# Kernel optimization log

Hardware: AMD Instinct MI355X
Metric: run time of the kernel (lower is better)

The kernel has to match this reference:

```python
import jax, jax.numpy as jnp
import numpy as np

N_NODES = 50000
N_EDGES = 1000000
NODE_IN = 64
EDGE_OUT = 64
NODE_OUT = 64
GLOBAL_DIM = 64
N_GRAPHS = 64


def _glorot(key, shape):
    fan_in = shape[0]
    return (jax.random.normal(key, shape, dtype=jnp.float32) / jnp.sqrt(jnp.float32(fan_in)))


def setup_inputs() -> dict:
    key = jax.random.key(0)
    ks = jax.random.split(key, 12)
    x = jax.random.normal(ks[0], (N_NODES, NODE_IN), dtype=jnp.float32)
    edge_index = jax.random.randint(ks[1], (2, N_EDGES), 0, N_NODES, dtype=jnp.int64 if jax.config.jax_enable_x64 else jnp.int32)
    edge_attr = jax.random.normal(ks[2], (N_EDGES, EDGE_OUT), dtype=jnp.float32)
    u = jax.random.normal(ks[3], (N_GRAPHS, GLOBAL_DIM), dtype=jnp.float32)
    batch = jnp.sort(jax.random.randint(ks[4], (N_NODES,), 0, N_GRAPHS, dtype=jnp.int64 if jax.config.jax_enable_x64 else jnp.int32))
    # node_mlp_1: Linear(node_in+edge_out -> node_out), ReLU, Linear(node_out -> node_out)
    W1 = _glorot(ks[5], (NODE_IN + EDGE_OUT, NODE_OUT))
    b1 = jnp.zeros((NODE_OUT,), dtype=jnp.float32)
    W2 = _glorot(ks[6], (NODE_OUT, NODE_OUT))
    b2 = jnp.zeros((NODE_OUT,), dtype=jnp.float32)
    # node_mlp_2: Linear(global_dim+node_in+node_out -> node_out), ReLU, Linear(node_out -> node_out)
    W3 = _glorot(ks[7], (GLOBAL_DIM + NODE_IN + NODE_OUT, NODE_OUT))
    b3 = jnp.zeros((NODE_OUT,), dtype=jnp.float32)
    W4 = _glorot(ks[8], (NODE_OUT, NODE_OUT))
    b4 = jnp.zeros((NODE_OUT,), dtype=jnp.float32)
    return {"x": x, "edge_index": edge_index, "edge_attr": edge_attr, "u": u, "batch": batch,
            "W1": W1, "b1": b1, "W2": W2, "b2": b2, "W3": W3, "b3": b3, "W4": W4, "b4": b4}


def reference(x, edge_index, edge_attr, u, batch, W1, b1, W2, b2, W3, b3, W4, b4):
    row, col = edge_index[0], edge_index[1]
    # per-edge MLP on [x[row] || edge_attr]  -> [E, node_out]
    e = jnp.concatenate([x[row], edge_attr], axis=1)
    e = jnp.maximum(e @ W1 + b1, 0.0) @ W2 + b2
    # scatter_mean over destination nodes (zero where a node has no incoming edges)
    sums = jax.ops.segment_sum(e, col, num_segments=N_NODES)
    counts = jax.ops.segment_sum(jnp.ones((e.shape[0],), dtype=e.dtype), col, num_segments=N_NODES)
    agg = sums / jnp.clip(counts, 1.0)[:, None]
    # per-node MLP on [x || agg || u[batch]]
    h = jnp.concatenate([x, agg, u[batch]], axis=1)
    return jnp.maximum(h @ W3 + b3, 0.0) @ W4 + b4
```

## Files before the change

kernel.cpp:

```cpp
#include <hip/hip_runtime.h>

#define E_TOTAL 1000000
#define NN 50000
#define NB_SCAN ((NN + 255) / 256)

typedef __attribute__((ext_vector_type(8))) short bf16x8;
typedef __attribute__((ext_vector_type(8))) __bf16 bfv8;
typedef __attribute__((ext_vector_type(4))) float f32x4;
typedef __attribute__((ext_vector_type(8))) unsigned short u16x8;

__device__ __forceinline__ float bf2f(unsigned short u) {
  unsigned int x = ((unsigned int)u) << 16;
  return __builtin_bit_cast(float, x);
}

__device__ __forceinline__ unsigned short f2bf(float v) {
  __bf16 b = (__bf16)v;
  return __builtin_bit_cast(unsigned short, b);
}

__device__ __forceinline__ bf16x8 pack8(float4 u, float4 v) {
  bfv8 f;
  f[0] = (__bf16)u.x; f[1] = (__bf16)u.y; f[2] = (__bf16)u.z; f[3] = (__bf16)u.w;
  f[4] = (__bf16)v.x; f[5] = (__bf16)v.y; f[6] = (__bf16)v.z; f[7] = (__bf16)v.w;
  return __builtin_bit_cast(bf16x8, f);
}

__device__ __forceinline__ bf16x8 cvt8(const float* __restrict__ p) {
  return pack8(*reinterpret_cast<const float4*>(p), *reinterpret_cast<const float4*>(p + 4));
}

__device__ __forceinline__ bf16x8 cvt8s(const float* __restrict__ p, float s) {
  const float4 v0 = *reinterpret_cast<const float4*>(p);
  const float4 v1 = *reinterpret_cast<const float4*>(p + 4);
  bfv8 f;
  f[0] = (__bf16)(v0.x * s); f[1] = (__bf16)(v0.y * s); f[2] = (__bf16)(v0.z * s); f[3] = (__bf16)(v0.w * s);
  f[4] = (__bf16)(v1.x * s); f[5] = (__bf16)(v1.y * s); f[6] = (__bf16)(v1.z * s); f[7] = (__bf16)(v1.w * s);
  return __builtin_bit_cast(bf16x8, f);
}


__global__ void count_kernel(const int* __restrict__ ei, float* __restrict__ counts) {
  int i = blockIdx.x * blockDim.x + threadIdx.x;
  if (i < E_TOTAL) atomicAdd(counts + ei[E_TOTAL + i], 1.0f);
}

__global__ void hist_kernel(const int* __restrict__ ei, int* __restrict__ cnt) {
  int i = blockIdx.x * blockDim.x + threadIdx.x;
  if (i < E_TOTAL) atomicAdd(cnt + ei[E_TOTAL + i], 1);
}

__global__ void scan_block_kernel(const int* __restrict__ cnt, int* __restrict__ offs,
                                  int* __restrict__ btot) {
  __shared__ int s[256];
  const int tid = threadIdx.x;
  const int i = blockIdx.x * 256 + tid;
  int v = (i < NN) ? cnt[i] : 0;
  s[tid] = v;
  __syncthreads();
#pragma unroll
  for (int d = 1; d < 256; d <<= 1) {
    int t = (tid >= d) ? s[tid - d] : 0;
    __syncthreads();
    s[tid] += t;
    __syncthreads();
  }
  int incl = s[tid];
  if (i < NN) offs[i] = incl - v;
  if (tid == 255) btot[blockIdx.x] = incl;
}

__global__ void scan_add_kernel(int* __restrict__ offs, const int* __restrict__ btot,
                                int* __restrict__ run) {
  __shared__ int s[256];
  const int tid = threadIdx.x, bid = blockIdx.x;
  s[tid] = (tid < bid && tid < NB_SCAN) ? btot[tid] : 0;
  __syncthreads();
#pragma unroll
  for (int d = 128; d > 0; d >>= 1) {
    if (tid < d) s[tid] += s[tid + d];
    __syncthreads();
  }
  const int base = s[0];
  const int i = bid * 256 + tid;
  if (i < NN) {
    int o = offs[i] + base;
    offs[i] = o;
    run[i] = o;
  }
  if (i == 0) offs[NN] = E_TOTAL;
}

template <int MODE>
__global__ __launch_bounds__(512) void edge_kernel(
    const float* __restrict__ x, const int* __restrict__ ei,
    const float* __restrict__ ea, const float* __restrict__ W1,
    const float* __restrict__ b1, const float* __restrict__ W2,
    const float* __restrict__ b2, float* __restrict__ sums,
    unsigned short* __restrict__ hbuf, int* __restrict__ run) {
  __shared__ unsigned short wlds[24 * 512];
  __shared__ unsigned short h_lds[8][16 * 72];
  const int tid = threadIdx.x;
  const int w = tid >> 6, l = tid & 63;
  const int c = l & 15, g = l >> 4;

  for (int idx = tid; idx < 16 * 512; idx += 512) {
    const int e = idx & 7, ll = (idx >> 3) & 63, ft = idx >> 9;
    const int s = ft >> 2, t = ft & 3;
    wlds[idx] = f2bf(W1[(s * 32 + (ll >> 4) * 8 + e) * 64 + t * 16 + (ll & 15)]);
  }
  for (int idx = tid; idx < 8 * 512; idx += 512) {
    const int e = idx & 7, ll = (idx >> 3) & 63, ft = idx >> 9;
    const int s = ft >> 2, t = ft & 3;
    wlds[16 * 512 + idx] = f2bf(W2[(s * 32 + (ll >> 4) * 8 + e) * 64 + t * 16 + (ll & 15)]);
  }
  __syncthreads();

  const int ebase0 = blockIdx.x * 512 + w * 64;
  if (ebase0 >= E_TOTAL) return;

  float b1v[4], b2v[4];
#pragma unroll
  for (int t = 0; t < 4; ++t) {
    b1v[t] = b1[t * 16 + c];
    b2v[t] = b2[t * 16 + c];
  }
  unsigned short* hl = h_lds[w];

  int idxc = ei[ebase0 + c];
  int colc = (MODE == 1) ? ei[E_TOTAL + ebase0 + c] : 0;
  const float* xp0 = x + (long)idxc * 64 + g * 8;
  const float* ap0 = ea + (long)(ebase0 + c) * 64 + g * 8;
  float4 xc0 = *reinterpret_cast<const float4*>(xp0);
  float4 xc1 = *reinterpret_cast<const float4*>(xp0 + 4);
  float4 xc2 = *reinterpret_cast<const float4*>(xp0 + 32);
  float4 xc3 = *reinterpret_cast<const float4*>(xp0 + 36);
  float4 ac0 = *reinterpret_cast<const float4*>(ap0);
  float4 ac1 = *reinterpret_cast<const float4*>(ap0 + 4);
  float4 ac2 = *reinterpret_cast<const float4*>(ap0 + 32);
  float4 ac3 = *reinterpret_cast<const float4*>(ap0 + 36);

#pragma unroll 1
  for (int it = 0; it < 4; ++it) {
    const int ebc = ebase0 + it * 16;
    const bool hasnext = (it < 3);

    int posc = 0;
    if (MODE == 1 && g == 0) posc = atomicAdd(run + colc, 1);

    bf16x8 a0 = pack8(xc0, xc1);
    bf16x8 a1 = pack8(xc2, xc3);
    bf16x8 a2 = pack8(ac0, ac1);
    bf16x8 a3 = pack8(ac2, ac3);

    int idxn = 0, coln = 0;
    float4 an0, an1, an2, an3, xn0, xn1, xn2, xn3;
    if (hasnext) {
      idxn = ei[ebc + 16 + c];
      if (MODE == 1) coln = ei[E_TOTAL + ebc + 16 + c];
      const float* apn = ea + (long)(ebc + 16 + c) * 64 + g * 8;
      an0 = *reinterpret_cast<const float4*>(apn);
      an1 = *reinterpret_cast<const float4*>(apn + 4);
      an2 = *reinterpret_cast<const float4*>(apn + 32);
      an3 = *reinterpret_cast<const float4*>(apn + 36);
    }

    f32x4 acc[4];
#pragma unroll
    for (int t = 0; t < 4; ++t) acc[t] = (f32x4){0.f, 0.f, 0.f, 0.f};
#pragma unroll
    for (int t = 0; t < 4; ++t) {
      bf16x8 wf0 = *reinterpret_cast<const bf16x8*>(wlds + ((0 * 4 + t) * 64 + l) * 8);
      bf16x8 wf1 = *reinterpret_cast<const bf16x8*>(wlds + ((1 * 4 + t) * 64 + l) * 8);
      bf16x8 wf2 = *reinterpret_cast<const bf16x8*>(wlds + ((2 * 4 + t) * 64 + l) * 8);
      bf16x8 wf3 = *reinterpret_cast<const bf16x8*>(wlds + ((3 * 4 + t) * 64 + l) * 8);
      acc[t] = __builtin_amdgcn_mfma_f32_16x16x32_bf16(a0, wf0, acc[t], 0, 0, 0);
      acc[t] = __builtin_amdgcn_mfma_f32_16x16x32_bf16(a1, wf1, acc[t], 0, 0, 0);
      acc[t] = __builtin_amdgcn_mfma_f32_16x16x32_bf16(a2, wf2, acc[t], 0, 0, 0);
      acc[t] = __builtin_amdgcn_mfma_f32_16x16x32_bf16(a3, wf3, acc[t], 0, 0, 0);
    }

    if (hasnext) {
      const float* xpn = x + (long)idxn * 64 + g * 8;
      xn0 = *reinterpret_cast<const float4*>(xpn);
      xn1 = *reinterpret_cast<const float4*>(xpn + 4);
      xn2 = *reinterpret_cast<const float4*>(xpn + 32);
      xn3 = *reinterpret_cast<const float4*>(xpn + 36);
    }

#pragma unroll
    for (int t = 0; t < 4; ++t)
#pragma unroll
      for (int r = 0; r < 4; ++r)
        hl[(g * 4 + r) * 72 + t * 16 + c] = f2bf(fmaxf(acc[t][r] + b1v[t], 0.f));
    __builtin_amdgcn_wave_barrier();
    bf16x8 h0 = *reinterpret_cast<const bf16x8*>(hl + c * 72 + g * 8);
    bf16x8 h1 = *reinterpret_cast<const bf16x8*>(hl + c * 72 + 32 + g * 8);

    f32x4 o[4];
#pragma unroll
    for (int t = 0; t < 4; ++t) o[t] = (f32x4){0.f, 0.f, 0.f, 0.f};
#pragma unroll
    for (int t = 0; t < 4; ++t) {
      bf16x8 wf0 = *reinterpret_cast<const bf16x8*>(wlds + 16 * 512 + ((0 * 4 + t) * 64 + l) * 8);
      bf16x8 wf1 = *reinterpret_cast<const bf16x8*>(wlds + 16 * 512 + ((1 * 4 + t) * 64 + l) * 8);
      o[t] = __builtin_amdgcn_mfma_f32_16x16x32_bf16(h0, wf0, o[t], 0, 0, 0);
      o[t] = __builtin_amdgcn_mfma_f32_16x16x32_bf16(h1, wf1, o[t], 0, 0, 0);
    }
    __builtin_amdgcn_wave_barrier();

    if (MODE == 0) {
#pragma unroll
      for (int r = 0; r < 4; ++r) {
        const int node = ei[E_TOTAL + ebc + g * 4 + r];
#pragma unroll
        for (int t = 0; t < 4; ++t)
          atomicAdd(sums + (long)node * 64 + t * 16 + c, o[t][r] + b2v[t]);
      }
    } else {
#pragma unroll
      for (int t = 0; t < 4; ++t)
#pragma unroll
        for (int r = 0; r < 4; ++r)
          hl[(g * 4 + r) * 72 + t * 16 + c] = f2bf(o[t][r] + b2v[t]);
      __builtin_amdgcn_wave_barrier();
      {
        const int srow = l >> 2, k4 = l & 3;
        const int pos = __shfl(posc, srow);
        const unsigned short* src = hl + srow * 72 + k4 * 16;
        unsigned short* dst = hbuf + (size_t)pos * 64 + k4 * 16;
        u16x8 v0 = *reinterpret_cast<const u16x8*>(src);
        u16x8 v1 = *reinterpret_cast<const u16x8*>(src + 8);
        *reinterpret_cast<u16x8*>(dst) = v0;
        *reinterpret_cast<u16x8*>(dst + 8) = v1;
      }
      __builtin_amdgcn_wave_barrier();
    }

    if (hasnext) {
      xc0 = xn0; xc1 = xn1; xc2 = xn2; xc3 = xn3;
      ac0 = an0; ac1 = an1; ac2 = an2; ac3 = an3;
      colc = coln;
    }
  }
}

__global__ __launch_bounds__(256, 1) void reduce_kernel(
    const unsigned short* __restrict__ hbuf, const int* __restrict__ offs,
    float* __restrict__ out) {
  const int l = threadIdx.x & 63, w = threadIdx.x >> 6;
  const int n = blockIdx.x * 4 + w;
  if (n >= NN) return;
  const int start = offs[n], end = offs[n + 1];
  const int slot = l >> 3, ch8 = (l & 7) * 8;
  float acc[8];
#pragma unroll
  for (int k = 0; k < 8; ++k) acc[k] = 0.f;
  for (int j0 = start; j0 < end; j0 += 8) {
    const int j = j0 + slot;
    if (j < end) {
      u16x8 v = *reinterpret_cast<const u16x8*>(hbuf + (size_t)j * 64 + ch8);
#pragma unroll
      for (int k = 0; k < 8; ++k) acc[k] += bf2f(v[k]);
    }
  }
#pragma unroll
  for (int k = 0; k < 8; ++k) {
    float v = acc[k];
    v += __shfl_xor(v, 8);
    v += __shfl_xor(v, 16);
    v += __shfl_xor(v, 32);
    acc[k] = v;
  }
  if (l < 8) {
    const float inv = 1.0f / fmaxf((float)(end - start), 1.0f);
    float* op = out + (size_t)n * 64 + l * 8;
    float4 r0 = {acc[0] * inv, acc[1] * inv, acc[2] * inv, acc[3] * inv};
    float4 r1 = {acc[4] * inv, acc[5] * inv, acc[6] * inv, acc[7] * inv};
    *reinterpret_cast<float4*>(op) = r0;
    *reinterpret_cast<float4*>(op + 4) = r1;
  }
}

template <bool WITH_INV>
__global__ __launch_bounds__(256, 1) void node_kernel(
    const float* __restrict__ x, const int* __restrict__ batch,
    const float* __restrict__ u, const float* __restrict__ W3,
    const float* __restrict__ b3, const float* __restrict__ W4,
    const float* __restrict__ b4, const float* __restrict__ counts,
    float* __restrict__ out) {
  __shared__ unsigned short h_lds[4][16 * 72];
  const int tid = threadIdx.x;
  const int w = tid >> 6, l = tid & 63;
  const int c = l & 15, g = l >> 4;

  bf16x8 w3f[6][4];
#pragma unroll
  for (int s = 0; s < 6; ++s)
#pragma unroll
    for (int t = 0; t < 4; ++t) {
      const float* wp = W3 + (s * 32 + g * 8) * 64 + t * 16 + c;
      bfv8 f;
#pragma unroll
      for (int e = 0; e < 8; ++e) f[e] = (__bf16)wp[e * 64];
      w3f[s][t] = __builtin_bit_cast(bf16x8, f);
    }
  bf16x8 w4f[2][4];
#pragma unroll
  for (int s = 0; s < 2; ++s)
#pragma unroll
    for (int t = 0; t < 4; ++t) {
      const float* wp = W4 + (s * 32 + g * 8) * 64 + t * 16 + c;
      bfv8 f;
#pragma unroll
      for (int e = 0; e < 8; ++e) f[e] = (__bf16)wp[e * 64];
      w4f[s][t] = __builtin_bit_cast(bf16x8, f);
    }
  float b3v[4], b4v[4];
#pragma unroll
  for (int t = 0; t < 4; ++t) {
    b3v[t] = b3[t * 16 + c];
    b4v[t] = b4[t * 16 + c];
  }

  unsigned short* hl = h_lds[w];
  const int nbase0 = blockIdx.x * 256 + w * 64;
#pragma unroll 1
  for (int it = 0; it < 4; ++it) {
    const int nb = nbase0 + it * 16;
    if (nb >= NN) break;
    const int my_n = nb + c;
    const float* xp = x + (long)my_n * 64 + g * 8;
    const float* sp = out + (long)my_n * 64 + g * 8;
    const float* up = u + (long)batch[my_n] * 64 + g * 8;
    bf16x8 a0 = cvt8(xp);
    bf16x8 a1 = cvt8(xp + 32);
    bf16x8 a2, a3;
    if (WITH_INV) {
      const float inv = 1.0f / fmaxf(counts[my_n], 1.0f);
      a2 = cvt8s(sp, inv);
      a3 = cvt8s(sp + 32, inv);
    } else {
      a2 = cvt8(sp);
      a3 = cvt8(sp + 32);
    }
    bf16x8 a4 = cvt8(up);
    bf16x8 a5 = cvt8(up + 32);

    f32x4 acc[4];
#pragma unroll
    for (int t = 0; t < 4; ++t) acc[t] = (f32x4){0.f, 0.f, 0.f, 0.f};
#pragma unroll
    for (int t = 0; t < 4; ++t) {
      acc[t] = __builtin_amdgcn_mfma_f32_16x16x32_bf16(a0, w3f[0][t], acc[t], 0, 0, 0);
      acc[t] = __builtin_amdgcn_mfma_f32_16x16x32_bf16(a1, w3f[1][t], acc[t], 0, 0, 0);
      acc[t] = __builtin_amdgcn_mfma_f32_16x16x32_bf16(a2, w3f[2][t], acc[t], 0, 0, 0);
      acc[t] = __builtin_amdgcn_mfma_f32_16x16x32_bf16(a3, w3f[3][t], acc[t], 0, 0, 0);
      acc[t] = __builtin_amdgcn_mfma_f32_16x16x32_bf16(a4, w3f[4][t], acc[t], 0, 0, 0);
      acc[t] = __builtin_amdgcn_mfma_f32_16x16x32_bf16(a5, w3f[5][t], acc[t], 0, 0, 0);
    }
#pragma unroll
    for (int t = 0; t < 4; ++t)
#pragma unroll
      for (int r = 0; r < 4; ++r)
        hl[(g * 4 + r) * 72 + t * 16 + c] = f2bf(fmaxf(acc[t][r] + b3v[t], 0.f));
    __builtin_amdgcn_wave_barrier();
    bf16x8 h0 = *reinterpret_cast<const bf16x8*>(hl + c * 72 + g * 8);
    bf16x8 h1 = *reinterpret_cast<const bf16x8*>(hl + c * 72 + 32 + g * 8);
    f32x4 o[4];
#pragma unroll
    for (int t = 0; t < 4; ++t) o[t] = (f32x4){0.f, 0.f, 0.f, 0.f};
#pragma unroll
    for (int t = 0; t < 4; ++t) {
      o[t] = __builtin_amdgcn_mfma_f32_16x16x32_bf16(h0, w4f[0][t], o[t], 0, 0, 0);
      o[t] = __builtin_amdgcn_mfma_f32_16x16x32_bf16(h1, w4f[1][t], o[t], 0, 0, 0);
    }
    __builtin_amdgcn_wave_barrier();
#pragma unroll
    for (int r = 0; r < 4; ++r) {
      const int nrow = nb + g * 4 + r;
#pragma unroll
      for (int t = 0; t < 4; ++t)
        out[(long)nrow * 64 + t * 16 + c] = o[t][r] + b4v[t];
    }
  }
}

extern "C" void kernel_launch(void* const* d_in, const int* in_sizes, int n_in,
                              void* d_out, int out_size, void* d_ws, size_t ws_size,
                              hipStream_t stream) {
  const float* x = (const float*)d_in[0];
  const int* ei = (const int*)d_in[1];
  const float* ea = (const float*)d_in[2];
  const float* u = (const float*)d_in[3];
  const int* batch = (const int*)d_in[4];
  const float* W1 = (const float*)d_in[5];
  const float* b1 = (const float*)d_in[6];
  const float* W2 = (const float*)d_in[7];
  const float* b2 = (const float*)d_in[8];
  const float* W3 = (const float*)d_in[9];
  const float* b3 = (const float*)d_in[10];
  const float* W4 = (const float*)d_in[11];
  const float* b4 = (const float*)d_in[12];
  float* out = (float*)d_out;

  const size_t HB_OFF = 0;
  const size_t OFFS_OFF = 128000000;
  const size_t RUN_OFF = 128400000;
  const size_t BTOT_OFF = 128800000;
  const size_t NEED = 128900000;

  const int egrid = (E_TOTAL + 255) / 256;
  const int egrid512 = (E_TOTAL + 511) / 512;
  const int ngrid = (NN + 255) / 256;

  if (ws_size >= NEED) {
    unsigned short* hbuf = (unsigned short*)((char*)d_ws + HB_OFF);
    int* offs = (int*)((char*)d_ws + OFFS_OFF);
    int* run = (int*)((char*)d_ws + RUN_OFF);
    int* btot = (int*)((char*)d_ws + BTOT_OFF);

    hipMemsetAsync(run, 0, (size_t)NN * sizeof(int), stream);
    hist_kernel<<<egrid, 256, 0, stream>>>(ei, run);
    scan_block_kernel<<<NB_SCAN, 256, 0, stream>>>(run, offs, btot);
    scan_add_kernel<<<NB_SCAN, 256, 0, stream>>>(offs, btot, run);
    edge_kernel<1><<<egrid512, 512, 0, stream>>>(x, ei, ea, W1, b1, W2, b2, nullptr, hbuf, run);
    reduce_kernel<<<(NN + 3) / 4, 256, 0, stream>>>(hbuf, offs, out);
    node_kernel<false><<<ngrid, 256, 0, stream>>>(x, batch, u, W3, b3, W4, b4, nullptr, out);
  } else {
    float* counts = (float*)d_ws;
    hipMemsetAsync(out, 0, (size_t)NN * 64 * sizeof(float), stream);
    hipMemsetAsync(counts, 0, (size_t)NN * sizeof(float), stream);
    count_kernel<<<egrid, 256, 0, stream>>>(ei, counts);
    edge_kernel<0><<<egrid512, 512, 0, stream>>>(x, ei, ea, W1, b1, W2, b2, out, nullptr, nullptr);
    node_kernel<true><<<ngrid, 256, 0, stream>>>(x, batch, u, W3, b3, W4, b4, counts, out);
  }
}
```

Before: 228.0 us.

## Sort edges by destination and reduce runs in-register before atomic scatter

Edges are counting-sorted by destination into a compact struct array (src, edge id, dst), and the edge MLP then processes edges in sorted order. Same-destination edges are summed in registers, with a whole-wave shortcut when all 16 rows share a node, before fp32 atomics into a sums buffer. This removes the 128MB bf16 per-edge intermediate buffer and the separate reduce kernel. The cost is a scatter kernel, gathered (non-contiguous) edge_attr reads, and remaining atomics, and accumulation order now varies between runs.

```diff
diff --git a/kernel.cpp b/kernel.cpp
--- a/kernel.cpp
+++ b/kernel.cpp
@@ -7,12 +7,6 @@
 typedef __attribute__((ext_vector_type(8))) short bf16x8;
 typedef __attribute__((ext_vector_type(8))) __bf16 bfv8;
 typedef __attribute__((ext_vector_type(4))) float f32x4;
-typedef __attribute__((ext_vector_type(8))) unsigned short u16x8;
-
-__device__ __forceinline__ float bf2f(unsigned short u) {
-  unsigned int x = ((unsigned int)u) << 16;
-  return __builtin_bit_cast(float, x);
-}
 
 __device__ __forceinline__ unsigned short f2bf(float v) {
   __bf16 b = (__bf16)v;
@@ -39,11 +33,6 @@
   return __builtin_bit_cast(bf16x8, f);
 }
 
-
-__global__ void count_kernel(const int* __restrict__ ei, float* __restrict__ counts) {
-  int i = blockIdx.x * blockDim.x + threadIdx.x;
-  if (i < E_TOTAL) atomicAdd(counts + ei[E_TOTAL + i], 1.0f);
-}
 
 __global__ void hist_kernel(const int* __restrict__ ei, int* __restrict__ cnt) {
   int i = blockIdx.x * blockDim.x + threadIdx.x;
@@ -70,7 +59,7 @@
   if (tid == 255) btot[blockIdx.x] = incl;
 }
 
-__global__ void scan_add_kernel(int* __restrict__ offs, const int* __restrict__ btot,
+__global__ void scan_add_kernel(const int* __restrict__ offs_in, const int* __restrict__ btot,
                                 int* __restrict__ run) {
   __shared__ int s[256];
   const int tid = threadIdx.x, bid = blockIdx.x;
@@ -83,21 +72,25 @@
   }
   const int base = s[0];
   const int i = bid * 256 + tid;
-  if (i < NN) {
-    int o = offs[i] + base;
-    offs[i] = o;
-    run[i] = o;
-  }
-  if (i == 0) offs[NN] = E_TOTAL;
-}
-
-template <int MODE>
+  if (i < NN) run[i] = offs_in[i] + base;
+}
+
+__global__ void scatter_kernel(const int* __restrict__ ei, int* __restrict__ run,
+                               int4* __restrict__ structs) {
+  int i = blockIdx.x * blockDim.x + threadIdx.x;
+  if (i < E_TOTAL) {
+    const int src = ei[i];
+    const int dst = ei[E_TOTAL + i];
+    const int pos = atomicAdd(run + dst, 1);
+    structs[pos] = (int4){src, i, dst, 0};
+  }
+}
+
 __global__ __launch_bounds__(512) void edge_kernel(
-    const float* __restrict__ x, const int* __restrict__ ei,
+    const float* __restrict__ x, const int4* __restrict__ structs,
     const float* __restrict__ ea, const float* __restrict__ W1,
     const float* __restrict__ b1, const float* __restrict__ W2,
-    const float* __restrict__ b2, float* __restrict__ sums,
-    unsigned short* __restrict__ hbuf, int* __restrict__ run) {
+    const float* __restrict__ b2, float* __restrict__ sums) {
   __shared__ unsigned short wlds[24 * 512];
   __shared__ unsigned short h_lds[8][16 * 72];
   const int tid = threadIdx.x;
@@ -127,10 +120,14 @@
   }
   unsigned short* hl = h_lds[w];
 
-  int idxc = ei[ebase0 + c];
-  int colc = (MODE == 1) ? ei[E_TOTAL + ebase0 + c] : 0;
-  const float* xp0 = x + (long)idxc * 64 + g * 8;
-  const float* ap0 = ea + (long)(ebase0 + c) * 64 + g * 8;
+  int4 s0 = structs[ebase0 + c];
+  int4 s1 = structs[ebase0 + 16 + c];
+  {
+    const float* xp0 = x + (long)s0.x * 64 + g * 8;
+    const float* ap0 = ea + (long)s0.y * 64 + g * 8;
+  }
+  const float* xp0 = x + (long)s0.x * 64 + g * 8;
+  const float* ap0 = ea + (long)s0.y * 64 + g * 8;
   float4 xc0 = *reinterpret_cast<const float4*>(xp0);
   float4 xc1 = *reinterpret_cast<const float4*>(xp0 + 4);
   float4 xc2 = *reinterpret_cast<const float4*>(xp0 + 32);
@@ -145,25 +142,21 @@
     const int ebc = ebase0 + it * 16;
     const bool hasnext = (it < 3);
 
-    int posc = 0;
-    if (MODE == 1 && g == 0) posc = atomicAdd(run + colc, 1);
+    int4 s2 = (int4){0, 0, 0, 0};
+    float4 an0, an1, an2, an3, xn0, xn1, xn2, xn3;
+    if (hasnext) {
+      const float* apn = ea + (long)s1.y * 64 + g * 8;
+      an0 = *reinterpret_cast<const float4*>(apn);
+      an1 = *reinterpret_cast<const float4*>(apn + 4);
+      an2 = *reinterpret_cast<const float4*>(apn + 32);
+      an3 = *reinterpret_cast<const float4*>(apn + 36);
+      if (it < 2) s2 = structs[ebc + 32 + c];
+    }
 
     bf16x8 a0 = pack8(xc0, xc1);
     bf16x8 a1 = pack8(xc2, xc3);
     bf16x8 a2 = pack8(ac0, ac1);
     bf16x8 a3 = pack8(ac2, ac3);
-
-    int idxn = 0, coln = 0;
-    float4 an0, an1, an2, an3, xn0, xn1, xn2, xn3;
-    if (hasnext) {
-      idxn = ei[ebc + 16 + c];
-      if (MODE == 1) coln = ei[E_TOTAL + ebc + 16 + c];
-      const float* apn = ea + (long)(ebc + 16 + c) * 64 + g * 8;
-      an0 = *reinterpret_cast<const float4*>(apn);
-      an1 = *reinterpret_cast<const float4*>(apn + 4);
-      an2 = *reinterpret_cast<const float4*>(apn + 32);
-      an3 = *reinterpret_cast<const float4*>(apn + 36);
-    }
 
     f32x4 acc[4];
 #pragma unroll
@@ -181,7 +174,7 @@
     }
 
     if (hasnext) {
-      const float* xpn = x + (long)idxn * 64 + g * 8;
+      const float* xpn = x + (long)s1.x * 64 + g * 8;
       xn0 = *reinterpret_cast<const float4*>(xpn);
       xn1 = *reinterpret_cast<const float4*>(xpn + 4);
       xn2 = *reinterpret_cast<const float4*>(xpn + 32);
@@ -208,87 +201,55 @@
       o[t] = __builtin_amdgcn_mfma_f32_16x16x32_bf16(h1, wf1, o[t], 0, 0, 0);
     }
     __builtin_amdgcn_wave_barrier();
-
-    if (MODE == 0) {
-#pragma unroll
-      for (int r = 0; r < 4; ++r) {
-        const int node = ei[E_TOTAL + ebc + g * 4 + r];
-#pragma unroll
-        for (int t = 0; t < 4; ++t)
-          atomicAdd(sums + (long)node * 64 + t * 16 + c, o[t][r] + b2v[t]);
+#pragma unroll
+    for (int t = 0; t < 4; ++t)
+#pragma unroll
+      for (int r = 0; r < 4; ++r) o[t][r] += b2v[t];
+
+    const int d0 = __shfl(s0.z, 0);
+    const bool uni = __all(s0.z == d0);
+    if (uni) {
+#pragma unroll
+      for (int t = 0; t < 4; ++t) {
+        float s = o[t][0] + o[t][1] + o[t][2] + o[t][3];
+        s += __shfl_xor(s, 16);
+        s += __shfl_xor(s, 32);
+        if (l < 16) atomicAdd(sums + (long)d0 * 64 + t * 16 + c, s);
       }
     } else {
-#pragma unroll
-      for (int t = 0; t < 4; ++t)
-#pragma unroll
-        for (int r = 0; r < 4; ++r)
-          hl[(g * 4 + r) * 72 + t * 16 + c] = f2bf(o[t][r] + b2v[t]);
-      __builtin_amdgcn_wave_barrier();
-      {
-        const int srow = l >> 2, k4 = l & 3;
-        const int pos = __shfl(posc, srow);
-        const unsigned short* src = hl + srow * 72 + k4 * 16;
-        unsigned short* dst = hbuf + (size_t)pos * 64 + k4 * 16;
-        u16x8 v0 = *reinterpret_cast<const u16x8*>(src);
-        u16x8 v1 = *reinterpret_cast<const u16x8*>(src + 8);
-        *reinterpret_cast<u16x8*>(dst) = v0;
-        *reinterpret_cast<u16x8*>(dst + 8) = v1;
+      int n0 = __shfl(s0.z, 4 * g + 0);
+      int n1 = __shfl(s0.z, 4 * g + 1);
+      int n2 = __shfl(s0.z, 4 * g + 2);
+      int n3 = __shfl(s0.z, 4 * g + 3);
+#pragma unroll
+      for (int t = 0; t < 4; ++t) {
+        const int chb = t * 16 + c;
+        float acc2 = o[t][0];
+        int cur = n0;
+        if (n1 == cur) acc2 += o[t][1];
+        else { atomicAdd(sums + (long)cur * 64 + chb, acc2); acc2 = o[t][1]; cur = n1; }
+        if (n2 == cur) acc2 += o[t][2];
+        else { atomicAdd(sums + (long)cur * 64 + chb, acc2); acc2 = o[t][2]; cur = n2; }
+        if (n3 == cur) acc2 += o[t][3];
+        else { atomicAdd(sums + (long)cur * 64 + chb, acc2); acc2 = o[t][3]; cur = n3; }
+        atomicAdd(sums + (long)cur * 64 + chb, acc2);
       }
-      __builtin_amdgcn_wave_barrier();
     }
 
     if (hasnext) {
       xc0 = xn0; xc1 = xn1; xc2 = xn2; xc3 = xn3;
       ac0 = an0; ac1 = an1; ac2 = an2; ac3 = an3;
-      colc = coln;
-    }
-  }
-}
-
-__global__ __launch_bounds__(256, 1) void reduce_kernel(
-    const unsigned short* __restrict__ hbuf, const int* __restrict__ offs,
-    float* __restrict__ out) {
-  const int l = threadIdx.x & 63, w = threadIdx.x >> 6;
-  const int n = blockIdx.x * 4 + w;
-  if (n >= NN) return;
-  const int start = offs[n], end = offs[n + 1];
-  const int slot = l >> 3, ch8 = (l & 7) * 8;
-  float acc[8];
-#pragma unroll
-  for (int k = 0; k < 8; ++k) acc[k] = 0.f;
-  for (int j0 = start; j0 < end; j0 += 8) {
-    const int j = j0 + slot;
-    if (j < end) {
-      u16x8 v = *reinterpret_cast<const u16x8*>(hbuf + (size_t)j * 64 + ch8);
-#pragma unroll
-      for (int k = 0; k < 8; ++k) acc[k] += bf2f(v[k]);
-    }
-  }
-#pragma unroll
-  for (int k = 0; k < 8; ++k) {
-    float v = acc[k];
-    v += __shfl_xor(v, 8);
-    v += __shfl_xor(v, 16);
-    v += __shfl_xor(v, 32);
-    acc[k] = v;
-  }
-  if (l < 8) {
-    const float inv = 1.0f / fmaxf((float)(end - start), 1.0f);
-    float* op = out + (size_t)n * 64 + l * 8;
-    float4 r0 = {acc[0] * inv, acc[1] * inv, acc[2] * inv, acc[3] * inv};
-    float4 r1 = {acc[4] * inv, acc[5] * inv, acc[6] * inv, acc[7] * inv};
-    *reinterpret_cast<float4*>(op) = r0;
-    *reinterpret_cast<float4*>(op + 4) = r1;
-  }
-}
-
-template <bool WITH_INV>
+      s0 = s1; s1 = s2;
+    }
+  }
+}
+
 __global__ __launch_bounds__(256, 1) void node_kernel(
     const float* __restrict__ x, const int* __restrict__ batch,
     const float* __restrict__ u, const float* __restrict__ W3,
     const float* __restrict__ b3, const float* __restrict__ W4,
-    const float* __restrict__ b4, const float* __restrict__ counts,
-    float* __restrict__ out) {
+    const float* __restrict__ b4, const int* __restrict__ cnt,
+    const float* __restrict__ sums, float* __restrict__ out) {
   __shared__ unsigned short h_lds[4][16 * 72];
   const int tid = threadIdx.x;
   const int w = tid >> 6, l = tid & 63;
@@ -331,19 +292,13 @@
     if (nb >= NN) break;
     const int my_n = nb + c;
     const float* xp = x + (long)my_n * 64 + g * 8;
-    const float* sp = out + (long)my_n * 64 + g * 8;
+    const float* sp = sums + (long)my_n * 64 + g * 8;
     const float* up = u + (long)batch[my_n] * 64 + g * 8;
+    const float inv = 1.0f / fmaxf((float)cnt[my_n], 1.0f);
     bf16x8 a0 = cvt8(xp);
     bf16x8 a1 = cvt8(xp + 32);
-    bf16x8 a2, a3;
-    if (WITH_INV) {
-      const float inv = 1.0f / fmaxf(counts[my_n], 1.0f);
-      a2 = cvt8s(sp, inv);
-      a3 = cvt8s(sp + 32, inv);
-    } else {
-      a2 = cvt8(sp);
-      a3 = cvt8(sp + 32);
-    }
+    bf16x8 a2 = cvt8s(sp, inv);
+    bf16x8 a3 = cvt8s(sp + 32, inv);
     bf16x8 a4 = cvt8(up);
     bf16x8 a5 = cvt8(up + 32);
 
@@ -404,35 +359,30 @@
   const float* b4 = (const float*)d_in[12];
   float* out = (float*)d_out;
 
-  const size_t HB_OFF = 0;
-  const size_t OFFS_OFF = 128000000;
-  const size_t RUN_OFF = 128400000;
-  const size_t BTOT_OFF = 128800000;
-  const size_t NEED = 128900000;
+  const size_t ST_OFF = 0;
+  const size_t SUM_OFF = 16000000;
+  const size_t CNT_OFF = 28800000;
+  const size_t RUN_OFF = 29000000;
+  const size_t OFFS_OFF = 29200000;
+  const size_t BTOT_OFF = 29400000;
+
+  int4* structs = (int4*)((char*)d_ws + ST_OFF);
+  float* sums = (float*)((char*)d_ws + SUM_OFF);
+  int* cnt = (int*)((char*)d_ws + CNT_OFF);
+  int* run = (int*)((char*)d_ws + RUN_OFF);
+  int* offs = (int*)((char*)d_ws + OFFS_OFF);
+  int* btot = (int*)((char*)d_ws + BTOT_OFF);
 
   const int egrid = (E_TOTAL + 255) / 256;
   const int egrid512 = (E_TOTAL + 511) / 512;
   const int ngrid = (NN + 255) / 256;
 
-  if (ws_size >= NEED) {
-    unsigned short* hbuf = (unsigned short*)((char*)d_ws + HB_OFF);
-    int* offs = (int*)((char*)d_ws + OFFS_OFF);
-    int* run = (int*)((char*)d_ws + RUN_OFF);
-    int* btot = (int*)((char*)d_ws + BTOT_OFF);
-
-    hipMemsetAsync(run, 0, (size_t)NN * sizeof(int), stream);
-    hist_kernel<<<egrid, 256, 0, stream>>>(ei, run);
-    scan_block_kernel<<<NB_SCAN, 256, 0, stream>>>(run, offs, btot);
-    scan_add_kernel<<<NB_SCAN, 256, 0, stream>>>(offs, btot, run);
-    edge_kernel<1><<<egrid512, 512, 0, stream>>>(x, ei, ea, W1, b1, W2, b2, nullptr, hbuf, run);
-    reduce_kernel<<<(NN + 3) / 4, 256, 0, stream>>>(hbuf, offs, out);
-    node_kernel<false><<<ngrid, 256, 0, stream>>>(x, batch, u, W3, b3, W4, b4, nullptr, out);
-  } else {
-    float* counts = (float*)d_ws;
-    hipMemsetAsync(out, 0, (size_t)NN * 64 * sizeof(float), stream);
-    hipMemsetAsync(counts, 0, (size_t)NN * sizeof(float), stream);
-    count_kernel<<<egrid, 256, 0, stream>>>(ei, counts);
-    edge_kernel<0><<<egrid512, 512, 0, stream>>>(x, ei, ea, W1, b1, W2, b2, out, nullptr, nullptr);
-    node_kernel<true><<<ngrid, 256, 0, stream>>>(x, batch, u, W3, b3, W4, b4, counts, out);
-  }
-}
+  hipMemsetAsync(cnt, 0, (size_t)NN * sizeof(int), stream);
+  hipMemsetAsync(sums, 0, (size_t)NN * 64 * sizeof(float), stream);
+  hist_kernel<<<egrid, 256, 0, stream>>>(ei, cnt);
+  scan_block_kernel<<<NB_SCAN, 256, 0, stream>>>(cnt, offs, btot);
+  scan_add_kernel<<<NB_SCAN, 256, 0, stream>>>(offs, btot, run);
+  scatter_kernel<<<egrid, 256, 0, stream>>>(ei, run, structs);
+  edge_kernel<<<egrid512, 512, 0, stream>>>(x, structs, ea, W1, b1, W2, b2, sums);
+  node_kernel<<<ngrid, 256, 0, stream>>>(x, batch, u, W3, b3, W4, b4, cnt, sums, out);
+}
```

New measurement: 322.3 us. 1.41x slower.

## Fold edge second linear layer into node MLP weights, pre-convert x to bf16

Applied to the files above, without the earlier changes.

Because scatter-mean is linear, the second edge-MLP layer (W2, b2) is moved after aggregation. It is folded into W3 as W2·W3 plus a bias term that is applied only to nodes with incoming edges. The edge kernel now writes ReLU(first-layer) activations straight to the sorted buffer, which removes the second MFMA pass and the LDS round trip. A small kernel pre-converts x to bf16 to halve gather traffic. The code also drops the low-workspace fallback path and batches the atomic position reservation per wave. In exchange it adds two tiny launches and a precomputed weight product whose rounding differs slightly from the reference.

```diff
diff --git a/kernel.cpp b/kernel.cpp
--- a/kernel.cpp
+++ b/kernel.cpp
@@ -7,6 +7,7 @@
 typedef __attribute__((ext_vector_type(8))) short bf16x8;
 typedef __attribute__((ext_vector_type(8))) __bf16 bfv8;
 typedef __attribute__((ext_vector_type(4))) float f32x4;
+typedef __attribute__((ext_vector_type(4))) unsigned short u16x4;
 typedef __attribute__((ext_vector_type(8))) unsigned short u16x8;
 
 __device__ __forceinline__ float bf2f(unsigned short u) {
@@ -30,20 +31,37 @@
   return pack8(*reinterpret_cast<const float4*>(p), *reinterpret_cast<const float4*>(p + 4));
 }
 
-__device__ __forceinline__ bf16x8 cvt8s(const float* __restrict__ p, float s) {
-  const float4 v0 = *reinterpret_cast<const float4*>(p);
-  const float4 v1 = *reinterpret_cast<const float4*>(p + 4);
-  bfv8 f;
-  f[0] = (__bf16)(v0.x * s); f[1] = (__bf16)(v0.y * s); f[2] = (__bf16)(v0.z * s); f[3] = (__bf16)(v0.w * s);
-  f[4] = (__bf16)(v1.x * s); f[5] = (__bf16)(v1.y * s); f[6] = (__bf16)(v1.z * s); f[7] = (__bf16)(v1.w * s);
-  return __builtin_bit_cast(bf16x8, f);
-}
-
-
-__global__ void count_kernel(const int* __restrict__ ei, float* __restrict__ counts) {
-  int i = blockIdx.x * blockDim.x + threadIdx.x;
-  if (i < E_TOTAL) atomicAdd(counts + ei[E_TOTAL + i], 1.0f);
-}
+__global__ void conv_kernel(const float* __restrict__ x, unsigned short* __restrict__ xb) {
+  const int i = blockIdx.x * 256 + threadIdx.x;
+  if (i < NN * 8) {
+    const float4 v0 = *reinterpret_cast<const float4*>(x + (size_t)i * 8);
+    const float4 v1 = *reinterpret_cast<const float4*>(x + (size_t)i * 8 + 4);
+    bf16x8 p = pack8(v0, v1);
+    *reinterpret_cast<bf16x8*>(xb + (size_t)i * 8) = p;
+  }
+}
+
+__global__ void w3p_kernel(const float* __restrict__ W2, const float* __restrict__ W3,
+                           const float* __restrict__ b2, float* __restrict__ W3p,
+                           float* __restrict__ bb) {
+  const int idx = blockIdx.x * 256 + threadIdx.x;
+  if (idx < 64 * 64) {
+    const int i = idx >> 6, j = idx & 63;
+    float s = 0.f;
+#pragma unroll 8
+    for (int k = 0; k < 64; ++k) s += W2[i * 64 + k] * W3[(64 + k) * 64 + j];
+    W3p[(64 + i) * 64 + j] = s;
+    W3p[i * 64 + j] = W3[i * 64 + j];
+    W3p[(128 + i) * 64 + j] = W3[(128 + i) * 64 + j];
+  } else if (idx < 64 * 64 + 64) {
+    const int j = idx - 64 * 64;
+    float s = 0.f;
+#pragma unroll 8
+    for (int k = 0; k < 64; ++k) s += b2[k] * W3[(64 + k) * 64 + j];
+    bb[j] = s;
+  }
+}
+
 
 __global__ void hist_kernel(const int* __restrict__ ei, int* __restrict__ cnt) {
   int i = blockIdx.x * blockDim.x + threadIdx.x;
@@ -91,15 +109,12 @@
   if (i == 0) offs[NN] = E_TOTAL;
 }
 
-template <int MODE>
 __global__ __launch_bounds__(512) void edge_kernel(
-    const float* __restrict__ x, const int* __restrict__ ei,
+    const unsigned short* __restrict__ xb, const int* __restrict__ ei,
     const float* __restrict__ ea, const float* __restrict__ W1,
-    const float* __restrict__ b1, const float* __restrict__ W2,
-    const float* __restrict__ b2, float* __restrict__ sums,
-    unsigned short* __restrict__ hbuf, int* __restrict__ run) {
-  __shared__ unsigned short wlds[24 * 512];
-  __shared__ unsigned short h_lds[8][16 * 72];
+    const float* __restrict__ b1, unsigned short* __restrict__ hbuf,
+    int* __restrict__ run) {
+  __shared__ unsigned short wlds[16 * 512];
   const int tid = threadIdx.x;
   const int w = tid >> 6, l = tid & 63;
   const int c = l & 15, g = l >> 4;
@@ -109,32 +124,24 @@
     const int s = ft >> 2, t = ft & 3;
     wlds[idx] = f2bf(W1[(s * 32 + (ll >> 4) * 8 + e) * 64 + t * 16 + (ll & 15)]);
   }
-  for (int idx = tid; idx < 8 * 512; idx += 512) {
-    const int e = idx & 7, ll = (idx >> 3) & 63, ft = idx >> 9;
-    const int s = ft >> 2, t = ft & 3;
-    wlds[16 * 512 + idx] = f2bf(W2[(s * 32 + (ll >> 4) * 8 + e) * 64 + t * 16 + (ll & 15)]);
-  }
   __syncthreads();
 
   const int ebase0 = blockIdx.x * 512 + w * 64;
   if (ebase0 >= E_TOTAL) return;
 
-  float b1v[4], b2v[4];
-#pragma unroll
-  for (int t = 0; t < 4; ++t) {
-    b1v[t] = b1[t * 16 + c];
-    b2v[t] = b2[t * 16 + c];
-  }
-  unsigned short* hl = h_lds[w];
-
-  int idxc = ei[ebase0 + c];
-  int colc = (MODE == 1) ? ei[E_TOTAL + ebase0 + c] : 0;
-  const float* xp0 = x + (long)idxc * 64 + g * 8;
+  const int idx_all = ei[ebase0 + l];
+  const int col_all = ei[E_TOTAL + ebase0 + l];
+  const int pos_all = atomicAdd(run + col_all, 1);
+
+  float b1v[4];
+#pragma unroll
+  for (int t = 0; t < 4; ++t) b1v[t] = b1[t * 16 + c];
+
+  int idxc = __shfl(idx_all, c);
+  const unsigned short* xp0 = xb + (size_t)idxc * 64 + g * 8;
+  bf16x8 xa0 = *reinterpret_cast<const bf16x8*>(xp0);
+  bf16x8 xa1 = *reinterpret_cast<const bf16x8*>(xp0 + 32);
   const float* ap0 = ea + (long)(ebase0 + c) * 64 + g * 8;
-  float4 xc0 = *reinterpret_cast<const float4*>(xp0);
-  float4 xc1 = *reinterpret_cast<const float4*>(xp0 + 4);
-  float4 xc2 = *reinterpret_cast<const float4*>(xp0 + 32);
-  float4 xc3 = *reinterpret_cast<const float4*>(xp0 + 36);
   float4 ac0 = *reinterpret_cast<const float4*>(ap0);
   float4 ac1 = *reinterpret_cast<const float4*>(ap0 + 4);
   float4 ac2 = *reinterpret_cast<const float4*>(ap0 + 32);
@@ -145,19 +152,10 @@
     const int ebc = ebase0 + it * 16;
     const bool hasnext = (it < 3);
 
-    int posc = 0;
-    if (MODE == 1 && g == 0) posc = atomicAdd(run + colc, 1);
-
-    bf16x8 a0 = pack8(xc0, xc1);
-    bf16x8 a1 = pack8(xc2, xc3);
-    bf16x8 a2 = pack8(ac0, ac1);
-    bf16x8 a3 = pack8(ac2, ac3);
-
-    int idxn = 0, coln = 0;
-    float4 an0, an1, an2, an3, xn0, xn1, xn2, xn3;
+    float4 an0, an1, an2, an3;
+    int idxn = 0;
     if (hasnext) {
-      idxn = ei[ebc + 16 + c];
-      if (MODE == 1) coln = ei[E_TOTAL + ebc + 16 + c];
+      idxn = __shfl(idx_all, (it + 1) * 16 + c);
       const float* apn = ea + (long)(ebc + 16 + c) * 64 + g * 8;
       an0 = *reinterpret_cast<const float4*>(apn);
       an1 = *reinterpret_cast<const float4*>(apn + 4);
@@ -165,6 +163,9 @@
       an3 = *reinterpret_cast<const float4*>(apn + 36);
     }
 
+    bf16x8 a2 = pack8(ac0, ac1);
+    bf16x8 a3 = pack8(ac2, ac3);
+
     f32x4 acc[4];
 #pragma unroll
     for (int t = 0; t < 4; ++t) acc[t] = (f32x4){0.f, 0.f, 0.f, 0.f};
@@ -174,73 +175,31 @@
       bf16x8 wf1 = *reinterpret_cast<const bf16x8*>(wlds + ((1 * 4 + t) * 64 + l) * 8);
       bf16x8 wf2 = *reinterpret_cast<const bf16x8*>(wlds + ((2 * 4 + t) * 64 + l) * 8);
       bf16x8 wf3 = *reinterpret_cast<const bf16x8*>(wlds + ((3 * 4 + t) * 64 + l) * 8);
-      acc[t] = __builtin_amdgcn_mfma_f32_16x16x32_bf16(a0, wf0, acc[t], 0, 0, 0);
-      acc[t] = __builtin_amdgcn_mfma_f32_16x16x32_bf16(a1, wf1, acc[t], 0, 0, 0);
+      acc[t] = __builtin_amdgcn_mfma_f32_16x16x32_bf16(xa0, wf0, acc[t], 0, 0, 0);
+      acc[t] = __builtin_amdgcn_mfma_f32_16x16x32_bf16(xa1, wf1, acc[t], 0, 0, 0);
       acc[t] = __builtin_amdgcn_mfma_f32_16x16x32_bf16(a2, wf2, acc[t], 0, 0, 0);
       acc[t] = __builtin_amdgcn_mfma_f32_16x16x32_bf16(a3, wf3, acc[t], 0, 0, 0);
     }
 
+    bf16x8 xan0, xan1;
     if (hasnext) {
-      const float* xpn = x + (long)idxn * 64 + g * 8;
-      xn0 = *reinterpret_cast<const float4*>(xpn);
-      xn1 = *reinterpret_cast<const float4*>(xpn + 4);
-      xn2 = *reinterpret_cast<const float4*>(xpn + 32);
-      xn3 = *reinterpret_cast<const float4*>(xpn + 36);
-    }
-
-#pragma unroll
-    for (int t = 0; t < 4; ++t)
-#pragma unroll
-      for (int r = 0; r < 4; ++r)
-        hl[(g * 4 + r) * 72 + t * 16 + c] = f2bf(fmaxf(acc[t][r] + b1v[t], 0.f));
-    __builtin_amdgcn_wave_barrier();
-    bf16x8 h0 = *reinterpret_cast<const bf16x8*>(hl + c * 72 + g * 8);
-    bf16x8 h1 = *reinterpret_cast<const bf16x8*>(hl + c * 72 + 32 + g * 8);
-
-    f32x4 o[4];
-#pragma unroll
-    for (int t = 0; t < 4; ++t) o[t] = (f32x4){0.f, 0.f, 0.f, 0.f};
-#pragma unroll
-    for (int t = 0; t < 4; ++t) {
-      bf16x8 wf0 = *reinterpret_cast<const bf16x8*>(wlds + 16 * 512 + ((0 * 4 + t) * 64 + l) * 8);
-      bf16x8 wf1 = *reinterpret_cast<const bf16x8*>(wlds + 16 * 512 + ((1 * 4 + t) * 64 + l) * 8);
-      o[t] = __builtin_amdgcn_mfma_f32_16x16x32_bf16(h0, wf0, o[t], 0, 0, 0);
-      o[t] = __builtin_amdgcn_mfma_f32_16x16x32_bf16(h1, wf1, o[t], 0, 0, 0);
-    }
-    __builtin_amdgcn_wave_barrier();
-
-    if (MODE == 0) {
-#pragma unroll
-      for (int r = 0; r < 4; ++r) {
-        const int node = ei[E_TOTAL + ebc + g * 4 + r];
-#pragma unroll
-        for (int t = 0; t < 4; ++t)
-          atomicAdd(sums + (long)node * 64 + t * 16 + c, o[t][r] + b2v[t]);
-      }
-    } else {
-#pragma unroll
-      for (int t = 0; t < 4; ++t)
-#pragma unroll
-        for (int r = 0; r < 4; ++r)
-          hl[(g * 4 + r) * 72 + t * 16 + c] = f2bf(o[t][r] + b2v[t]);
-      __builtin_amdgcn_wave_barrier();
-      {
-        const int srow = l >> 2, k4 = l & 3;
-        const int pos = __shfl(posc, srow);
-        const unsigned short* src = hl + srow * 72 + k4 * 16;
-        unsigned short* dst = hbuf + (size_t)pos * 64 + k4 * 16;
-        u16x8 v0 = *reinterpret_cast<const u16x8*>(src);
-        u16x8 v1 = *reinterpret_cast<const u16x8*>(src + 8);
-        *reinterpret_cast<u16x8*>(dst) = v0;
-        *reinterpret_cast<u16x8*>(dst + 8) = v1;
-      }
-      __builtin_amdgcn_wave_barrier();
+      const unsigned short* xpn = xb + (size_t)idxn * 64 + g * 8;
+      xan0 = *reinterpret_cast<const bf16x8*>(xpn);
+      xan1 = *reinterpret_cast<const bf16x8*>(xpn + 32);
+    }
+
+#pragma unroll
+    for (int r = 0; r < 4; ++r) {
+      const int pos = __shfl(pos_all, it * 16 + g * 4 + r);
+      u16x4 vv;
+#pragma unroll
+      for (int t = 0; t < 4; ++t) vv[t] = f2bf(fmaxf(acc[t][r] + b1v[t], 0.f));
+      *reinterpret_cast<u16x4*>(hbuf + (size_t)pos * 64 + c * 4) = vv;
     }
 
     if (hasnext) {
-      xc0 = xn0; xc1 = xn1; xc2 = xn2; xc3 = xn3;
+      xa0 = xan0; xa1 = xan1;
       ac0 = an0; ac1 = an1; ac2 = an2; ac3 = an3;
-      colc = coln;
     }
   }
 }
@@ -252,14 +211,14 @@
   const int n = blockIdx.x * 4 + w;
   if (n >= NN) return;
   const int start = offs[n], end = offs[n + 1];
-  const int slot = l >> 3, ch8 = (l & 7) * 8;
+  const int slot = l >> 3, p8 = (l & 7) * 8;
   float acc[8];
 #pragma unroll
   for (int k = 0; k < 8; ++k) acc[k] = 0.f;
   for (int j0 = start; j0 < end; j0 += 8) {
     const int j = j0 + slot;
     if (j < end) {
-      u16x8 v = *reinterpret_cast<const u16x8*>(hbuf + (size_t)j * 64 + ch8);
+      u16x8 v = *reinterpret_cast<const u16x8*>(hbuf + (size_t)j * 64 + p8);
 #pragma unroll
       for (int k = 0; k < 8; ++k) acc[k] += bf2f(v[k]);
     }
@@ -274,21 +233,21 @@
   }
   if (l < 8) {
     const float inv = 1.0f / fmaxf((float)(end - start), 1.0f);
-    float* op = out + (size_t)n * 64 + l * 8;
-    float4 r0 = {acc[0] * inv, acc[1] * inv, acc[2] * inv, acc[3] * inv};
-    float4 r1 = {acc[4] * inv, acc[5] * inv, acc[6] * inv, acc[7] * inv};
-    *reinterpret_cast<float4*>(op) = r0;
-    *reinterpret_cast<float4*>(op + 4) = r1;
-  }
-}
-
-template <bool WITH_INV>
+#pragma unroll
+    for (int j = 0; j < 8; ++j) {
+      const int p = l * 8 + j;
+      const int ch = (p & 3) * 16 + (p >> 2);
+      out[(size_t)n * 64 + ch] = acc[j] * inv;
+    }
+  }
+}
+
 __global__ __launch_bounds__(256, 1) void node_kernel(
-    const float* __restrict__ x, const int* __restrict__ batch,
-    const float* __restrict__ u, const float* __restrict__ W3,
+    const unsigned short* __restrict__ xb, const int* __restrict__ batch,
+    const float* __restrict__ u, const float* __restrict__ W3p,
     const float* __restrict__ b3, const float* __restrict__ W4,
-    const float* __restrict__ b4, const float* __restrict__ counts,
-    float* __restrict__ out) {
+    const float* __restrict__ b4, const float* __restrict__ bb,
+    const int* __restrict__ offs, float* __restrict__ out) {
   __shared__ unsigned short h_lds[4][16 * 72];
   const int tid = threadIdx.x;
   const int w = tid >> 6, l = tid & 63;
@@ -299,7 +258,7 @@
   for (int s = 0; s < 6; ++s)
 #pragma unroll
     for (int t = 0; t < 4; ++t) {
-      const float* wp = W3 + (s * 32 + g * 8) * 64 + t * 16 + c;
+      const float* wp = W3p + (s * 32 + g * 8) * 64 + t * 16 + c;
       bfv8 f;
 #pragma unroll
       for (int e = 0; e < 8; ++e) f[e] = (__bf16)wp[e * 64];
@@ -316,11 +275,12 @@
       for (int e = 0; e < 8; ++e) f[e] = (__bf16)wp[e * 64];
       w4f[s][t] = __builtin_bit_cast(bf16x8, f);
     }
-  float b3v[4], b4v[4];
+  float b3v[4], b4v[4], bbv[4];
 #pragma unroll
   for (int t = 0; t < 4; ++t) {
     b3v[t] = b3[t * 16 + c];
     b4v[t] = b4[t * 16 + c];
+    bbv[t] = bb[t * 16 + c];
   }
 
   unsigned short* hl = h_lds[w];
@@ -330,20 +290,14 @@
     const int nb = nbase0 + it * 16;
     if (nb >= NN) break;
     const int my_n = nb + c;
-    const float* xp = x + (long)my_n * 64 + g * 8;
     const float* sp = out + (long)my_n * 64 + g * 8;
     const float* up = u + (long)batch[my_n] * 64 + g * 8;
-    bf16x8 a0 = cvt8(xp);
-    bf16x8 a1 = cvt8(xp + 32);
-    bf16x8 a2, a3;
-    if (WITH_INV) {
-      const float inv = 1.0f / fmaxf(counts[my_n], 1.0f);
-      a2 = cvt8s(sp, inv);
-      a3 = cvt8s(sp + 32, inv);
-    } else {
-      a2 = cvt8(sp);
-      a3 = cvt8(sp + 32);
-    }
+    const float flag = (offs[my_n + 1] > offs[my_n]) ? 1.f : 0.f;
+    const unsigned short* xp = xb + (size_t)my_n * 64 + g * 8;
+    bf16x8 a0 = *reinterpret_cast<const bf16x8*>(xp);
+    bf16x8 a1 = *reinterpret_cast<const bf16x8*>(xp + 32);
+    bf16x8 a2 = cvt8(sp);
+    bf16x8 a3 = cvt8(sp + 32);
     bf16x8 a4 = cvt8(up);
     bf16x8 a5 = cvt8(up + 32);
 
@@ -358,6 +312,12 @@
       acc[t] = __builtin_amdgcn_mfma_f32_16x16x32_bf16(a3, w3f[3][t], acc[t], 0, 0, 0);
       acc[t] = __builtin_amdgcn_mfma_f32_16x16x32_bf16(a4, w3f[4][t], acc[t], 0, 0, 0);
       acc[t] = __builtin_amdgcn_mfma_f32_16x16x32_bf16(a5, w3f[5][t], acc[t], 0, 0, 0);
+    }
+#pragma unroll
+    for (int r = 0; r < 4; ++r) {
+      const float fr = __shfl(flag, g * 4 + r);
+#pragma unroll
+      for (int t = 0; t < 4; ++t) acc[t][r] += fr * bbv[t];
     }
 #pragma unroll
     for (int t = 0; t < 4; ++t)
@@ -408,31 +368,29 @@
   const size_t OFFS_OFF = 128000000;
   const size_t RUN_OFF = 128400000;
   const size_t BTOT_OFF = 128800000;
-  const size_t NEED = 128900000;
+  const size_t W3P_OFF = 128804096;
+  const size_t BB_OFF = 128853248;
+  const size_t XB_OFF = 128900000;
+
+  unsigned short* hbuf = (unsigned short*)((char*)d_ws + HB_OFF);
+  int* offs = (int*)((char*)d_ws + OFFS_OFF);
+  int* run = (int*)((char*)d_ws + RUN_OFF);
+  int* btot = (int*)((char*)d_ws + BTOT_OFF);
+  float* W3p = (float*)((char*)d_ws + W3P_OFF);
+  float* bbv = (float*)((char*)d_ws + BB_OFF);
+  unsigned short* xbp = (unsigned short*)((char*)d_ws + XB_OFF);
 
   const int egrid = (E_TOTAL + 255) / 256;
   const int egrid512 = (E_TOTAL + 511) / 512;
   const int ngrid = (NN + 255) / 256;
 
-  if (ws_size >= NEED) {
-    unsigned short* hbuf = (unsigned short*)((char*)d_ws + HB_OFF);
-    int* offs = (int*)((char*)d_ws + OFFS_OFF);
-    int* run = (int*)((char*)d_ws + RUN_OFF);
-    int* btot = (int*)((char*)d_ws + BTOT_OFF);
-
-    hipMemsetAsync(run, 0, (size_t)NN * sizeof(int), stream);
-    hist_kernel<<<egrid, 256, 0, stream>>>(ei, run);
-    scan_block_kernel<<<NB_SCAN, 256, 0, stream>>>(run, offs, btot);
-    scan_add_kernel<<<NB_SCAN, 256, 0, stream>>>(offs, btot, run);
-    edge_kernel<1><<<egrid512, 512, 0, stream>>>(x, ei, ea, W1, b1, W2, b2, nullptr, hbuf, run);
-    reduce_kernel<<<(NN + 3) / 4, 256, 0, stream>>>(hbuf, offs, out);
-    node_kernel<false><<<ngrid, 256, 0, stream>>>(x, batch, u, W3, b3, W4, b4, nullptr, out);
-  } else {
-    float* counts = (float*)d_ws;
-    hipMemsetAsync(out, 0, (size_t)NN * 64 * sizeof(float), stream);
-    hipMemsetAsync(counts, 0, (size_t)NN * sizeof(float), stream);
-    count_kernel<<<egrid, 256, 0, stream>>>(ei, counts);
-    edge_kernel<0><<<egrid512, 512, 0, stream>>>(x, ei, ea, W1, b1, W2, b2, out, nullptr, nullptr);
-    node_kernel<true><<<ngrid, 256, 0, stream>>>(x, batch, u, W3, b3, W4, b4, counts, out);
-  }
-}
+  hipMemsetAsync(run, 0, (size_t)NN * sizeof(int), stream);
+  conv_kernel<<<(NN * 8 + 255) / 256, 256, 0, stream>>>(x, xbp);
+  w3p_kernel<<<(64 * 64 + 64 + 255) / 256, 256, 0, stream>>>(W2, W3, b2, W3p, bbv);
+  hist_kernel<<<egrid, 256, 0, stream>>>(ei, run);
+  scan_block_kernel<<<NB_SCAN, 256, 0, stream>>>(run, offs, btot);
+  scan_add_kernel<<<NB_SCAN, 256, 0, stream>>>(offs, btot, run);
+  edge_kernel<<<egrid512, 512, 0, stream>>>(xbp, ei, ea, W1, b1, hbuf, run);
+  reduce_kernel<<<(NN + 3) / 4, 256, 0, stream>>>(hbuf, offs, out);
+  node_kernel<<<ngrid, 256, 0, stream>>>(xbp, batch, u, W3p, b3, W4, b4, bbv, offs, out);
+}
```

Result: slower. 236.5 us (+3.7%).
